# Optimization experiments

Hardware: AMD Instinct MI355X
Metric: run time of the kernel (lower is better)

## Reference

```python
import jax, jax.numpy as jnp
import numpy as np

SPATIAL_W = 1.0
INTENSITY_W = 1.0
MAX_ITERS = 100
CONV_THRESH = 1e-4
BOUNDARY = 0.1
NUM_CLASSES = 2
DIRS = ((-1, 0), (1, 0), (0, -1), (0, 1))  # 4-neighborhood


def setup_inputs() -> dict:
    key = jax.random.key(0)
    k1, k2, k3 = jax.random.split(key, 3)
    H = W = 1024
    image = jax.random.uniform(k1, (H, W), dtype=jnp.float32)
    labels = jax.random.randint(k2, (H, W), 1, NUM_CLASSES + 1)
    u = jax.random.uniform(k3, (H, W))
    seeds = jnp.where(u < 0.002, labels, 0).astype(jnp.int32)
    # guarantee both classes present (torch code maps sorted unique labels -> class idx)
    seeds = seeds.at[0, 0].set(1).at[0, 1].set(2)
    return {"image": image, "seeds": seeds}


def _shift(x, di, dj):
    """out[i, j] = x[i+di, j+dj] if in-bounds else 0. Static di, dj in {-1,0,1}."""
    H, W = x.shape[0], x.shape[1]
    pad = [(1, 1), (1, 1)] + [(0, 0)] * (x.ndim - 2)
    xp = jnp.pad(x, pad)
    return xp[1 + di:1 + di + H, 1 + dj:1 + dj + W]


def _transition_stencil(image):
    """Row-normalized 4-neighbor transition weights, [4, H, W].
    Equivalent to the dense NxN matrix P of the torch code restricted to its
    nonzero 4-neighbor stencil."""
    img = image[..., None]  # [H, W, 1] (grayscale -> C=1)
    ones = jnp.ones(image.shape, image.dtype)
    ws = []
    for di, dj in DIRS:
        valid = _shift(ones, di, dj)              # 1 where neighbor in-bounds
        nb = _shift(img, di, dj)                   # neighbor pixel values
        same = ((img > BOUNDARY) ^ (nb > BOUNDARY)).astype(image.dtype)
        diff = img - nb + same
        intensity = jnp.sqrt(jnp.sum(diff * diff, axis=-1))  # per-channel L2 norm
        dist = float(np.sqrt(di * di + dj * dj))  # == 1 for 4-neighborhood
        w = jnp.exp(-SPATIAL_W * dist) * jnp.exp(-INTENSITY_W * intensity) * valid
        ws.append(w)
    ws = jnp.stack(ws)  # [4, H, W]
    rowsum = jnp.sum(ws, axis=0)
    rowsum = jnp.where(rowsum == 0, jnp.ones_like(rowsum), rowsum)
    return ws / rowsum


def reference(image, seeds):
    P = _transition_stencil(image)  # [4, H, W]
    seed_mask = (seeds > 0)[..., None]  # [H, W, 1]
    # one-hot seed probabilities: label l -> class l-1 (sorted unique labels {1,2})
    init = jnp.stack([seeds == l for l in range(1, NUM_CLASSES + 1)],
                     axis=-1).astype(image.dtype)  # [H, W, C]

    def matvec(x):  # (P @ x) as a stencil: x is [H, W, C]
        out = jnp.zeros_like(x)
        for d, (di, dj) in enumerate(DIRS):
            out = out + P[d][..., None] * _shift(x, di, dj)
        return out

    def step(carry, _):
        x, done = carry
        new = jnp.where(seed_mask, init, matvec(x))  # seeds are absorbing
        d = jnp.linalg.norm(new - x)
        new = jnp.where(done, x, new)               # freeze after convergence
        done = done | (d < CONV_THRESH)
        return (new, done), None

    (x, _), _ = jax.lax.scan(step, (init, jnp.array(False)), None, length=MAX_ITERS)
    return x  # [H, W, NUM_CLASSES]
```

## Files before the change

kernel.cpp:

```cpp
#include <hip/hip_runtime.h>
#include <hip/hip_fp16.h>

typedef __attribute__((ext_vector_type(2))) int i32x2;

#define HH 1024
#define ROWP 512
#define NBLK 256
#define TPB 512
#define NSYNC 50
#define BOUNDARY_F 0.1f
#define TOKEN 0x5A5A5A5Au

union h2u { __half2 h; int i; };

__device__ __forceinline__ i32x2 pack4(float4 v) {
    h2u a, b;
    a.h = __float22half2_rn(make_float2(v.x, v.y));
    b.h = __float22half2_rn(make_float2(v.z, v.w));
    i32x2 r; r.x = a.i; r.y = b.i;
    return r;
}
__device__ __forceinline__ float4 unpack4(i32x2 p) {
    h2u a, b; a.i = p.x; b.i = p.y;
    float2 lo = __half22float2(a.h);
    float2 hi = __half22float2(b.h);
    return make_float4(lo.x, lo.y, hi.x, hi.y);
}

__device__ __forceinline__ void cst8(i32x2* base, int elem, i32x2 val) {
    asm volatile("global_store_dwordx2 %0, %1, %2 sc0 sc1"
                 :: "v"(elem * 8), "v"(val), "s"(base) : "memory");
}
__device__ __forceinline__ i32x2 cld8(const i32x2* base, int elem) {
    i32x2 t;
    asm volatile("global_load_dwordx2 %0, %1, %2 sc0 sc1"
                 : "=v"(t) : "v"(elem * 8), "s"(base) : "memory");
    return t;
}
__device__ __forceinline__ void wait4(i32x2& a, i32x2& b, i32x2& c, i32x2& d) {
    asm volatile("s_waitcnt vmcnt(0)"
                 : "+v"(a), "+v"(b), "+v"(c), "+v"(d) :: "memory");
}
__device__ __forceinline__ void waitvm0() {
    asm volatile("s_waitcnt vmcnt(0)" ::: "memory");
}

__device__ __forceinline__ float wfun(float c, float n, float valid) {
    float same = ((c > BOUNDARY_F) != (n > BOUNDARY_F)) ? 1.0f : 0.0f;
    return valid * __expf(-fabsf(c - n + same));
}

__device__ __forceinline__ float4 stepr(const float* w, bool m0, bool m1,
                                        float4 xc, float4 xu, float4 xd,
                                        float2 xl, float2 xr) {
    float4 o;
    o.x = w[0]*xu.x + w[1]*xd.x + w[2]*xl.x + w[3]*xc.z;
    o.y = w[0]*xu.y + w[1]*xd.y + w[2]*xl.y + w[3]*xc.w;
    o.z = w[4]*xu.z + w[5]*xd.z + w[6]*xc.x + w[7]*xr.x;
    o.w = w[4]*xu.w + w[5]*xd.w + w[6]*xc.y + w[7]*xr.y;
    if (m0) { o.x = xc.x; o.y = xc.y; }
    if (m1) { o.z = xc.z; o.w = xc.w; }
    return o;
}

__device__ __forceinline__ void horiz(const float4* row, int tid, float4 xc,
                                      float2* xl, float2* xr) {
    const float2* r2 = (const float2*)row;
    *xl = (tid > 0) ? r2[2 * tid - 1] : make_float2(xc.x, xc.y);
    *xr = (tid < ROWP - 1) ? r2[2 * tid + 2] : make_float2(xc.z, xc.w);
}

__launch_bounds__(TPB)
__global__ void rw_persist_kernel(const float* __restrict__ img,
                                  const int* __restrict__ seeds,
                                  float4* __restrict__ out4,
                                  i32x2* __restrict__ parE,
                                  i32x2* __restrict__ parO,
                                  unsigned* __restrict__ flags) {
    const int tid = threadIdx.x;
    const int blk = blockIdx.x;
    const int band = ((blk & 7) << 5) | (blk >> 3);
    const int i0 = band * 4;

    __shared__ float4 srows[10][ROWP];

    float cfv[6][8];
    unsigned mb0 = 0, mb1 = 0;
    float4 s0, s1, s2, s3;
    {
        const float2* img2 = (const float2*)img;
        const int2* seeds2 = (const int2*)seeds;
#pragma unroll
        for (int L = 0; L < 6; ++L) {
            const int g = min(max(i0 - 1 + L, 0), HH - 1);
            const int P = g * ROWP + tid;
            const int p = P * 2;
            const int j = p & 1023;
            const int uP = (g > 0) ? P - ROWP : P;
            const int dP = (g < HH - 1) ? P + ROWP : P;
            const int lp = (j > 0) ? p - 1 : p;
            const int rp = (j < 1022) ? p + 2 : p + 1;

            float2 cc = img2[P], iu = img2[uP], id = img2[dP];
            float il = img[lp], ir = img[rp];
            const float vU = (g > 0) ? 1.0f : 0.0f;
            const float vD = (g < HH - 1) ? 1.0f : 0.0f;
            const float vL = (j > 0) ? 1.0f : 0.0f;
            const float vR = (j < 1022) ? 1.0f : 0.0f;

            float w0u = wfun(cc.x, iu.x, vU), w0d = wfun(cc.x, id.x, vD);
            float w0l = wfun(cc.x, il, vL),   w0r = wfun(cc.x, cc.y, 1.0f);
            float rs0 = w0u + w0d + w0l + w0r;
            float inv0 = (rs0 > 0.0f) ? 1.0f / rs0 : 0.0f;
            float w1u = wfun(cc.y, iu.y, vU), w1d = wfun(cc.y, id.y, vD);
            float w1l = wfun(cc.y, cc.x, 1.0f), w1r = wfun(cc.y, ir, vR);
            float rs1 = w1u + w1d + w1l + w1r;
            float inv1 = (rs1 > 0.0f) ? 1.0f / rs1 : 0.0f;

            cfv[L][0] = w0u * inv0; cfv[L][1] = w0d * inv0;
            cfv[L][2] = w0l * inv0; cfv[L][3] = w0r * inv0;
            cfv[L][4] = w1u * inv1; cfv[L][5] = w1d * inv1;
            cfv[L][6] = w1l * inv1; cfv[L][7] = w1r * inv1;

            int2 s = seeds2[P];
            if (s.x > 0) mb0 |= 1u << L;
            if (s.y > 0) mb1 |= 1u << L;
            if (L >= 1 && L <= 4) {
                float4 v;
                v.x = (s.x == 1) ? 1.0f : 0.0f;
                v.y = (s.x == 2) ? 1.0f : 0.0f;
                v.z = (s.y == 1) ? 1.0f : 0.0f;
                v.w = (s.y == 2) ? 1.0f : 0.0f;
                if (L == 1) s0 = v; else if (L == 2) s1 = v;
                else if (L == 3) s2 = v; else s3 = v;
            }
        }
    }

    srows[1][tid] = s0; srows[2][tid] = s1;
    srows[3][tid] = s2; srows[4][tid] = s3;
    cst8(parE, (i0 + 0) * ROWP + tid, pack4(s0));
    cst8(parE, (i0 + 1) * ROWP + tid, pack4(s1));
    cst8(parE, (i0 + 2) * ROWP + tid, pack4(s2));
    cst8(parE, (i0 + 3) * ROWP + tid, pack4(s3));
    waitvm0();
    __syncthreads();
    if (tid == 0)
        __hip_atomic_store(&flags[band], TOKEN, __ATOMIC_RELAXED,
                           __HIP_MEMORY_SCOPE_AGENT);

    const int gU2 = max(i0 - 2, 0), gU1 = max(i0 - 1, 0);
    const int gD0 = min(i0 + 4, HH - 1), gD1 = min(i0 + 5, HH - 1);

    for (int m = 0; m < NSYNC; ++m) {
        if (tid == 0 && band > 0) {
            int guard = 0;
            while (__hip_atomic_load(&flags[m * NBLK + band - 1], __ATOMIC_RELAXED,
                                     __HIP_MEMORY_SCOPE_AGENT) != TOKEN) {
                __builtin_amdgcn_s_sleep(1);
                if (++guard > (1 << 20)) break;
            }
        }
        if (tid == 64 && band < NBLK - 1) {
            int guard = 0;
            while (__hip_atomic_load(&flags[m * NBLK + band + 1], __ATOMIC_RELAXED,
                                     __HIP_MEMORY_SCOPE_AGENT) != TOKEN) {
                __builtin_amdgcn_s_sleep(1);
                if (++guard > (1 << 20)) break;
            }
        }
        __syncthreads();
        asm volatile("" ::: "memory");

        const i32x2* pin = (m & 1) ? parO : parE;

        i32x2 rA = cld8(pin, gU2 * ROWP + tid);
        i32x2 rB = cld8(pin, gU1 * ROWP + tid);
        i32x2 rC = cld8(pin, gD0 * ROWP + tid);
        i32x2 rD = cld8(pin, gD1 * ROWP + tid);

        float2 xl, xr;
        horiz(&srows[2][0], tid, s1, &xl, &xr);
        float4 y2 = stepr(cfv[2], (mb0 >> 2) & 1, (mb1 >> 2) & 1, s1, s0, s2, xl, xr);
        horiz(&srows[3][0], tid, s2, &xl, &xr);
        float4 y3 = stepr(cfv[3], (mb0 >> 3) & 1, (mb1 >> 3) & 1, s2, s1, s3, xl, xr);
        srows[7][tid] = y2;
        srows[8][tid] = y3;

        wait4(rA, rB, rC, rD);
        float4 vU2 = unpack4(rA);
        float4 vU1 = unpack4(rB);
        float4 vD0 = unpack4(rC);
        float4 vD1 = unpack4(rD);
        srows[0][tid] = vU1;
        srows[5][tid] = vD0;
        __syncthreads();

        horiz(&srows[0][0], tid, vU1, &xl, &xr);
        float4 y0 = stepr(cfv[0], (mb0 >> 0) & 1, (mb1 >> 0) & 1, vU1, vU2, s0, xl, xr);
        horiz(&srows[1][0], tid, s0, &xl, &xr);
        float4 y1 = stepr(cfv[1], (mb0 >> 1) & 1, (mb1 >> 1) & 1, s0, vU1, s1, xl, xr);
        horiz(&srows[4][0], tid, s3, &xl, &xr);
        float4 y4 = stepr(cfv[4], (mb0 >> 4) & 1, (mb1 >> 4) & 1, s3, s2, vD0, xl, xr);
        horiz(&srows[5][0], tid, vD0, &xl, &xr);
        float4 y5 = stepr(cfv[5], (mb0 >> 5) & 1, (mb1 >> 5) & 1, vD0, s3, vD1, xl, xr);
        srows[6][tid] = y1;
        srows[9][tid] = y4;
        __syncthreads();

        horiz(&srows[6][0], tid, y1, &xl, &xr);
        float4 o0 = stepr(cfv[1], (mb0 >> 1) & 1, (mb1 >> 1) & 1, y1, y0, y2, xl, xr);
        horiz(&srows[7][0], tid, y2, &xl, &xr);
        float4 o1 = stepr(cfv[2], (mb0 >> 2) & 1, (mb1 >> 2) & 1, y2, y1, y3, xl, xr);
        horiz(&srows[8][0], tid, y3, &xl, &xr);
        float4 o2 = stepr(cfv[3], (mb0 >> 3) & 1, (mb1 >> 3) & 1, y3, y2, y4, xl, xr);
        horiz(&srows[9][0], tid, y4, &xl, &xr);
        float4 o3 = stepr(cfv[4], (mb0 >> 4) & 1, (mb1 >> 4) & 1, y4, y3, y5, xl, xr);

        if (m == NSYNC - 1) {
            out4[(i0 + 0) * ROWP + tid] = o0;
            out4[(i0 + 1) * ROWP + tid] = o1;
            out4[(i0 + 2) * ROWP + tid] = o2;
            out4[(i0 + 3) * ROWP + tid] = o3;
            break;
        }

        i32x2* pout = (m & 1) ? parE : parO;
        srows[1][tid] = o0; srows[2][tid] = o1;
        srows[3][tid] = o2; srows[4][tid] = o3;
        cst8(pout, (i0 + 0) * ROWP + tid, pack4(o0));
        cst8(pout, (i0 + 1) * ROWP + tid, pack4(o1));
        cst8(pout, (i0 + 2) * ROWP + tid, pack4(o2));
        cst8(pout, (i0 + 3) * ROWP + tid, pack4(o3));
        s0 = o0; s1 = o1; s2 = o2; s3 = o3;
        waitvm0();
        __syncthreads();
        if (tid == 0)
            __hip_atomic_store(&flags[(m + 1) * NBLK + band], TOKEN,
                               __ATOMIC_RELAXED, __HIP_MEMORY_SCOPE_AGENT);
    }
}

extern "C" void kernel_launch(void* const* d_in, const int* in_sizes, int n_in,
                              void* d_out, int out_size, void* d_ws, size_t ws_size,
                              hipStream_t stream) {
    const float* img = (const float*)d_in[0];
    const int* seeds = (const int*)d_in[1];

    float4* out4 = (float4*)d_out;
    char* ws = (char*)d_ws;
    i32x2* parE = (i32x2*)ws;
    i32x2* parO = (i32x2*)(ws + 4ull * 1024 * 1024);
    unsigned* flags = (unsigned*)(ws + 8ull * 1024 * 1024);

    rw_persist_kernel<<<NBLK, TPB, 0, stream>>>(img, seeds, out4, parE, parO, flags);
}
```

Measured before the change: 250.8 us.

## Switch from row bands to 2D tiles with shared-memory state and halo exchange

The persistent kernel now splits the grid into 16x16 two-dimensional tiles of 64x32 pixel-pairs instead of 4-row full-width bands. Tile state, coefficients and seed masks live in shared memory, and only halo cells are exchanged through global buffers. Each block waits on up to eight neighbour flags per sync step, and a separate init kernel clears the flags. The aim is to shrink global halo traffic per step relative to interior work. The cost is more LDS traffic and more synchronisation dependencies, plus an extra kernel launch.

```diff
diff --git a/kernel.cpp b/kernel.cpp
--- a/kernel.cpp
+++ b/kernel.cpp
@@ -1,15 +1,22 @@
 #include <hip/hip_runtime.h>
 #include <hip/hip_fp16.h>
 
+typedef unsigned long long u64;
 typedef __attribute__((ext_vector_type(2))) int i32x2;
 
 #define HH 1024
-#define ROWP 512
-#define NBLK 256
+#define WP 512
 #define TPB 512
+#define NTX 16
+#define NTY 16
+#define NBLK (NTX * NTY)
+#define SR 68
+#define SP 34
+#define NCELL (SR * SP)
 #define NSYNC 50
 #define BOUNDARY_F 0.1f
 #define TOKEN 0x5A5A5A5Au
+#define FLAGS_N (NSYNC * NBLK)
 
 union h2u { __half2 h; int i; };
 
@@ -20,27 +27,20 @@
     i32x2 r; r.x = a.i; r.y = b.i;
     return r;
 }
-__device__ __forceinline__ float4 unpack4(i32x2 p) {
-    h2u a, b; a.i = p.x; b.i = p.y;
+__device__ __forceinline__ float4 unpack4u(u64 p) {
+    h2u a, b; a.i = (int)(unsigned)p; b.i = (int)(unsigned)(p >> 32);
     float2 lo = __half22float2(a.h);
     float2 hi = __half22float2(b.h);
     return make_float4(lo.x, lo.y, hi.x, hi.y);
 }
 
+__device__ __forceinline__ u64 cld(const u64* p) {
+    return __hip_atomic_load(p, __ATOMIC_RELAXED, __HIP_MEMORY_SCOPE_AGENT);
+}
 __device__ __forceinline__ void cst8(i32x2* base, int elem, i32x2 val) {
     asm volatile("global_store_dwordx2 %0, %1, %2 sc0 sc1"
                  :: "v"(elem * 8), "v"(val), "s"(base) : "memory");
 }
-__device__ __forceinline__ i32x2 cld8(const i32x2* base, int elem) {
-    i32x2 t;
-    asm volatile("global_load_dwordx2 %0, %1, %2 sc0 sc1"
-                 : "=v"(t) : "v"(elem * 8), "s"(base) : "memory");
-    return t;
-}
-__device__ __forceinline__ void wait4(i32x2& a, i32x2& b, i32x2& c, i32x2& d) {
-    asm volatile("s_waitcnt vmcnt(0)"
-                 : "+v"(a), "+v"(b), "+v"(c), "+v"(d) :: "memory");
-}
 __device__ __forceinline__ void waitvm0() {
     asm volatile("s_waitcnt vmcnt(0)" ::: "memory");
 }
@@ -50,63 +50,63 @@
     return valid * __expf(-fabsf(c - n + same));
 }
 
-__device__ __forceinline__ float4 stepr(const float* w, bool m0, bool m1,
-                                        float4 xc, float4 xu, float4 xd,
-                                        float2 xl, float2 xr) {
+__device__ __forceinline__ float4 upd2(float4 c0, float4 c1, unsigned char m,
+                                       float4 xc, float4 xu, float4 xd,
+                                       float2 xl, float2 xr) {
     float4 o;
-    o.x = w[0]*xu.x + w[1]*xd.x + w[2]*xl.x + w[3]*xc.z;
-    o.y = w[0]*xu.y + w[1]*xd.y + w[2]*xl.y + w[3]*xc.w;
-    o.z = w[4]*xu.z + w[5]*xd.z + w[6]*xc.x + w[7]*xr.x;
-    o.w = w[4]*xu.w + w[5]*xd.w + w[6]*xc.y + w[7]*xr.y;
-    if (m0) { o.x = xc.x; o.y = xc.y; }
-    if (m1) { o.z = xc.z; o.w = xc.w; }
+    o.x = c0.x*xu.x + c0.y*xd.x + c0.z*xl.x + c0.w*xc.z;
+    o.y = c0.x*xu.y + c0.y*xd.y + c0.z*xl.y + c0.w*xc.w;
+    o.z = c1.x*xu.z + c1.y*xd.z + c1.z*xc.x + c1.w*xr.x;
+    o.w = c1.x*xu.w + c1.y*xd.w + c1.z*xc.y + c1.w*xr.y;
+    if (m & 1) { o.x = xc.x; o.y = xc.y; }
+    if (m & 2) { o.z = xc.z; o.w = xc.w; }
     return o;
 }
 
-__device__ __forceinline__ void horiz(const float4* row, int tid, float4 xc,
-                                      float2* xl, float2* xr) {
-    const float2* r2 = (const float2*)row;
-    *xl = (tid > 0) ? r2[2 * tid - 1] : make_float2(xc.x, xc.y);
-    *xr = (tid < ROWP - 1) ? r2[2 * tid + 2] : make_float2(xc.z, xc.w);
+__global__ void rw_init_kernel(unsigned* __restrict__ flags) {
+    int g = blockIdx.x * blockDim.x + threadIdx.x;
+    if (g < FLAGS_N) flags[g] = 0u;
 }
 
 __launch_bounds__(TPB)
 __global__ void rw_persist_kernel(const float* __restrict__ img,
                                   const int* __restrict__ seeds,
                                   float4* __restrict__ out4,
-                                  i32x2* __restrict__ parE,
-                                  i32x2* __restrict__ parO,
+                                  u64* __restrict__ parE,
+                                  u64* __restrict__ parO,
                                   unsigned* __restrict__ flags) {
     const int tid = threadIdx.x;
     const int blk = blockIdx.x;
-    const int band = ((blk & 7) << 5) | (blk >> 3);
-    const int i0 = band * 4;
-
-    __shared__ float4 srows[10][ROWP];
-
-    float cfv[6][8];
-    unsigned mb0 = 0, mb1 = 0;
-    float4 s0, s1, s2, s3;
+    const int tx = blk & (NTX - 1), ty = blk >> 4;
+    const int row0 = ty * 64 - 2;
+    const int pr0  = tx * 32 - 1;
+
+    __shared__ float4 xs[SR][SP + 1];
+    __shared__ float4 cf0s[SR][SP];
+    __shared__ float4 cf1s[SR][SP];
+    __shared__ unsigned char msks[SR][SP + 2];
+
     {
         const float2* img2 = (const float2*)img;
         const int2* seeds2 = (const int2*)seeds;
-#pragma unroll
-        for (int L = 0; L < 6; ++L) {
-            const int g = min(max(i0 - 1 + L, 0), HH - 1);
-            const int P = g * ROWP + tid;
-            const int p = P * 2;
-            const int j = p & 1023;
-            const int uP = (g > 0) ? P - ROWP : P;
-            const int dP = (g < HH - 1) ? P + ROWP : P;
-            const int lp = (j > 0) ? p - 1 : p;
-            const int rp = (j < 1022) ? p + 2 : p + 1;
+        for (int c = tid; c < NCELL; c += TPB) {
+            const int r = c / SP, q = c - (c / SP) * SP;
+            const int gi = row0 + r;
+            const int gq = pr0 + q;
+            const int ci = min(max(gi, 0), HH - 1);
+            const int cq = min(max(gq, 0), WP - 1);
+            const int gj = 2 * gq;
+            const int P  = ci * WP + cq;
+            const int uP = max(ci - 1, 0) * WP + cq;
+            const int dP = min(ci + 1, HH - 1) * WP + cq;
 
             float2 cc = img2[P], iu = img2[uP], id = img2[dP];
-            float il = img[lp], ir = img[rp];
-            const float vU = (g > 0) ? 1.0f : 0.0f;
-            const float vD = (g < HH - 1) ? 1.0f : 0.0f;
-            const float vL = (j > 0) ? 1.0f : 0.0f;
-            const float vR = (j < 1022) ? 1.0f : 0.0f;
+            float il = img[max(2 * P - 1, 0)];
+            float ir = img[min(2 * P + 2, HH * 1024 - 1)];
+            const float vU = (gi > 0) ? 1.0f : 0.0f;
+            const float vD = (gi < HH - 1) ? 1.0f : 0.0f;
+            const float vL = (gj > 0) ? 1.0f : 0.0f;
+            const float vR = (gj < 1022) ? 1.0f : 0.0f;
 
             float w0u = wfun(cc.x, iu.x, vU), w0d = wfun(cc.x, id.x, vD);
             float w0l = wfun(cc.x, il, vL),   w0r = wfun(cc.x, cc.y, 1.0f);
@@ -117,126 +117,142 @@
             float rs1 = w1u + w1d + w1l + w1r;
             float inv1 = (rs1 > 0.0f) ? 1.0f / rs1 : 0.0f;
 
-            cfv[L][0] = w0u * inv0; cfv[L][1] = w0d * inv0;
-            cfv[L][2] = w0l * inv0; cfv[L][3] = w0r * inv0;
-            cfv[L][4] = w1u * inv1; cfv[L][5] = w1d * inv1;
-            cfv[L][6] = w1l * inv1; cfv[L][7] = w1r * inv1;
+            cf0s[r][q] = make_float4(w0u*inv0, w0d*inv0, w0l*inv0, w0r*inv0);
+            cf1s[r][q] = make_float4(w1u*inv1, w1d*inv1, w1l*inv1, w1r*inv1);
 
             int2 s = seeds2[P];
-            if (s.x > 0) mb0 |= 1u << L;
-            if (s.y > 0) mb1 |= 1u << L;
-            if (L >= 1 && L <= 4) {
-                float4 v;
-                v.x = (s.x == 1) ? 1.0f : 0.0f;
-                v.y = (s.x == 2) ? 1.0f : 0.0f;
-                v.z = (s.y == 1) ? 1.0f : 0.0f;
-                v.w = (s.y == 2) ? 1.0f : 0.0f;
-                if (L == 1) s0 = v; else if (L == 2) s1 = v;
-                else if (L == 3) s2 = v; else s3 = v;
-            }
+            msks[r][q] = (unsigned char)((s.x > 0 ? 1 : 0) | (s.y > 0 ? 2 : 0));
+            xs[r][q] = make_float4((s.x == 1) ? 1.0f : 0.0f,
+                                   (s.x == 2) ? 1.0f : 0.0f,
+                                   (s.y == 1) ? 1.0f : 0.0f,
+                                   (s.y == 2) ? 1.0f : 0.0f);
         }
     }
-
-    srows[1][tid] = s0; srows[2][tid] = s1;
-    srows[3][tid] = s2; srows[4][tid] = s3;
-    cst8(parE, (i0 + 0) * ROWP + tid, pack4(s0));
-    cst8(parE, (i0 + 1) * ROWP + tid, pack4(s1));
-    cst8(parE, (i0 + 2) * ROWP + tid, pack4(s2));
-    cst8(parE, (i0 + 3) * ROWP + tid, pack4(s3));
-    waitvm0();
     __syncthreads();
-    if (tid == 0)
-        __hip_atomic_store(&flags[band], TOKEN, __ATOMIC_RELAXED,
-                           __HIP_MEMORY_SCOPE_AGENT);
-
-    const int gU2 = max(i0 - 2, 0), gU1 = max(i0 - 1, 0);
-    const int gD0 = min(i0 + 4, HH - 1), gD1 = min(i0 + 5, HH - 1);
+
+    int sr = 0, sq = 0;
+    const bool isStager = (tid < 264);
+    if (tid < 136) {
+        int k = tid / SP;
+        sr = (k < 2) ? k : 64 + k;
+        sq = tid - k * SP;
+    } else if (tid < 264) {
+        int j = tid - 136;
+        sr = 2 + (j >> 1);
+        sq = (j & 1) * 33;
+    }
+    const int sgi = min(max(row0 + sr, 0), HH - 1);
+    const int sgq = min(max(pr0 + sq, 0), WP - 1);
 
     for (int m = 0; m < NSYNC; ++m) {
-        if (tid == 0 && band > 0) {
-            int guard = 0;
-            while (__hip_atomic_load(&flags[m * NBLK + band - 1], __ATOMIC_RELAXED,
-                                     __HIP_MEMORY_SCOPE_AGENT) != TOKEN) {
-                __builtin_amdgcn_s_sleep(1);
-                if (++guard > (1 << 20)) break;
-            }
-        }
-        if (tid == 64 && band < NBLK - 1) {
-            int guard = 0;
-            while (__hip_atomic_load(&flags[m * NBLK + band + 1], __ATOMIC_RELAXED,
-                                     __HIP_MEMORY_SCOPE_AGENT) != TOKEN) {
-                __builtin_amdgcn_s_sleep(1);
-                if (++guard > (1 << 20)) break;
-            }
-        }
-        __syncthreads();
-        asm volatile("" ::: "memory");
-
-        const i32x2* pin = (m & 1) ? parO : parE;
-
-        i32x2 rA = cld8(pin, gU2 * ROWP + tid);
-        i32x2 rB = cld8(pin, gU1 * ROWP + tid);
-        i32x2 rC = cld8(pin, gD0 * ROWP + tid);
-        i32x2 rD = cld8(pin, gD1 * ROWP + tid);
-
-        float2 xl, xr;
-        horiz(&srows[2][0], tid, s1, &xl, &xr);
-        float4 y2 = stepr(cfv[2], (mb0 >> 2) & 1, (mb1 >> 2) & 1, s1, s0, s2, xl, xr);
-        horiz(&srows[3][0], tid, s2, &xl, &xr);
-        float4 y3 = stepr(cfv[3], (mb0 >> 3) & 1, (mb1 >> 3) & 1, s2, s1, s3, xl, xr);
-        srows[7][tid] = y2;
-        srows[8][tid] = y3;
-
-        wait4(rA, rB, rC, rD);
-        float4 vU2 = unpack4(rA);
-        float4 vU1 = unpack4(rB);
-        float4 vD0 = unpack4(rC);
-        float4 vD1 = unpack4(rD);
-        srows[0][tid] = vU1;
-        srows[5][tid] = vD0;
-        __syncthreads();
-
-        horiz(&srows[0][0], tid, vU1, &xl, &xr);
-        float4 y0 = stepr(cfv[0], (mb0 >> 0) & 1, (mb1 >> 0) & 1, vU1, vU2, s0, xl, xr);
-        horiz(&srows[1][0], tid, s0, &xl, &xr);
-        float4 y1 = stepr(cfv[1], (mb0 >> 1) & 1, (mb1 >> 1) & 1, s0, vU1, s1, xl, xr);
-        horiz(&srows[4][0], tid, s3, &xl, &xr);
-        float4 y4 = stepr(cfv[4], (mb0 >> 4) & 1, (mb1 >> 4) & 1, s3, s2, vD0, xl, xr);
-        horiz(&srows[5][0], tid, vD0, &xl, &xr);
-        float4 y5 = stepr(cfv[5], (mb0 >> 5) & 1, (mb1 >> 5) & 1, vD0, s3, vD1, xl, xr);
-        srows[6][tid] = y1;
-        srows[9][tid] = y4;
-        __syncthreads();
-
-        horiz(&srows[6][0], tid, y1, &xl, &xr);
-        float4 o0 = stepr(cfv[1], (mb0 >> 1) & 1, (mb1 >> 1) & 1, y1, y0, y2, xl, xr);
-        horiz(&srows[7][0], tid, y2, &xl, &xr);
-        float4 o1 = stepr(cfv[2], (mb0 >> 2) & 1, (mb1 >> 2) & 1, y2, y1, y3, xl, xr);
-        horiz(&srows[8][0], tid, y3, &xl, &xr);
-        float4 o2 = stepr(cfv[3], (mb0 >> 3) & 1, (mb1 >> 3) & 1, y3, y2, y4, xl, xr);
-        horiz(&srows[9][0], tid, y4, &xl, &xr);
-        float4 o3 = stepr(cfv[4], (mb0 >> 4) & 1, (mb1 >> 4) & 1, y4, y3, y5, xl, xr);
+        u64 stg = 0;
+        if (m > 0) {
+            if (tid < 8) {
+                const int dy[8] = {-1, 1, 0, 0, -1, -1, 1, 1};
+                const int dx[8] = {0, 0, -1, 1, -1, 1, -1, 1};
+                int nty = ty + dy[tid], ntx = tx + dx[tid];
+                if (nty >= 0 && nty < NTY && ntx >= 0 && ntx < NTX) {
+                    const int fi = m * NBLK + nty * NTX + ntx;
+                    int guard = 0;
+                    while (__hip_atomic_load(&flags[fi], __ATOMIC_RELAXED,
+                                             __HIP_MEMORY_SCOPE_AGENT) != TOKEN) {
+                        __builtin_amdgcn_s_sleep(1);
+                        if (++guard > (1 << 20)) break;
+                    }
+                }
+            }
+            __syncthreads();
+            asm volatile("" ::: "memory");
+            const u64* pin = (m & 1) ? parO : parE;
+            if (isStager) stg = cld(&pin[sgi * WP + sgq]);
+        }
+
+        float4 yA[4];
+#pragma unroll
+        for (int k = 0; k < 4; ++k) {
+            int idx = tid + k * TPB;
+            if (idx < 1860) {
+                int r = 3 + idx / 30, q = 2 + idx % 30;
+                float4 xc = xs[r][q];
+                float2 xl = make_float2(xs[r][q - 1].z, xs[r][q - 1].w);
+                float2 xr = make_float2(xs[r][q + 1].x, xs[r][q + 1].y);
+                yA[k] = upd2(cf0s[r][q], cf1s[r][q], msks[r][q],
+                             xc, xs[r - 1][q], xs[r + 1][q], xl, xr);
+            }
+        }
+        if (m > 0 && isStager) xs[sr][sq] = unpack4u(stg);
+        __syncthreads();
+
+        float4 yB;
+        int br = 1, bq = 0;
+        if (tid < 384) {
+            if (tid < 136) {
+                int k = tid / SP;
+                br = (k < 2) ? 1 + k : 63 + k;
+                bq = tid - k * SP;
+            } else {
+                int j = tid - 136;
+                br = 3 + (j >> 2);
+                const int QT[4] = {0, 1, 32, 33};
+                bq = QT[j & 3];
+            }
+            float4 xc = xs[br][bq];
+            float2 xl = (bq > 0) ? make_float2(xs[br][bq - 1].z, xs[br][bq - 1].w)
+                                 : make_float2(xc.x, xc.y);
+            float2 xr = (bq < SP - 1) ? make_float2(xs[br][bq + 1].x, xs[br][bq + 1].y)
+                                      : make_float2(xc.z, xc.w);
+            yB = upd2(cf0s[br][bq], cf1s[br][bq], msks[br][bq],
+                      xc, xs[br - 1][bq], xs[br + 1][bq], xl, xr);
+        }
+        __syncthreads();
+
+#pragma unroll
+        for (int k = 0; k < 4; ++k) {
+            int idx = tid + k * TPB;
+            if (idx < 1860) {
+                int r = 3 + idx / 30, q = 2 + idx % 30;
+                xs[r][q] = yA[k];
+            }
+        }
+        if (tid < 384) xs[br][bq] = yB;
+        __syncthreads();
+
+        float4 o[4];
+#pragma unroll
+        for (int k = 0; k < 4; ++k) {
+            int c = tid + k * TPB;
+            int r = 2 + (c >> 5), q = 1 + (c & 31);
+            float4 xc = xs[r][q];
+            float2 xl = make_float2(xs[r][q - 1].z, xs[r][q - 1].w);
+            float2 xr = make_float2(xs[r][q + 1].x, xs[r][q + 1].y);
+            o[k] = upd2(cf0s[r][q], cf1s[r][q], msks[r][q],
+                        xc, xs[r - 1][q], xs[r + 1][q], xl, xr);
+        }
 
         if (m == NSYNC - 1) {
-            out4[(i0 + 0) * ROWP + tid] = o0;
-            out4[(i0 + 1) * ROWP + tid] = o1;
-            out4[(i0 + 2) * ROWP + tid] = o2;
-            out4[(i0 + 3) * ROWP + tid] = o3;
+#pragma unroll
+            for (int k = 0; k < 4; ++k) {
+                int c = tid + k * TPB;
+                int r = 2 + (c >> 5), q = 1 + (c & 31);
+                out4[(row0 + r) * WP + (pr0 + q)] = o[k];
+            }
             break;
         }
 
-        i32x2* pout = (m & 1) ? parE : parO;
-        srows[1][tid] = o0; srows[2][tid] = o1;
-        srows[3][tid] = o2; srows[4][tid] = o3;
-        cst8(pout, (i0 + 0) * ROWP + tid, pack4(o0));
-        cst8(pout, (i0 + 1) * ROWP + tid, pack4(o1));
-        cst8(pout, (i0 + 2) * ROWP + tid, pack4(o2));
-        cst8(pout, (i0 + 3) * ROWP + tid, pack4(o3));
-        s0 = o0; s1 = o1; s2 = o2; s3 = o3;
+        __syncthreads();
+        i32x2* pout = (i32x2*)(((m + 1) & 1) ? parO : parE);
+#pragma unroll
+        for (int k = 0; k < 4; ++k) {
+            int c = tid + k * TPB;
+            int r = 2 + (c >> 5), q = 1 + (c & 31);
+            xs[r][q] = o[k];
+            if (r <= 3 || r >= 64 || q == 1 || q == 32)
+                cst8(pout, (row0 + r) * WP + (pr0 + q), pack4(o[k]));
+        }
         waitvm0();
         __syncthreads();
         if (tid == 0)
-            __hip_atomic_store(&flags[(m + 1) * NBLK + band], TOKEN,
+            __hip_atomic_store(&flags[(m + 1) * NBLK + blk], TOKEN,
                                __ATOMIC_RELAXED, __HIP_MEMORY_SCOPE_AGENT);
     }
 }
@@ -249,9 +265,10 @@
 
     float4* out4 = (float4*)d_out;
     char* ws = (char*)d_ws;
-    i32x2* parE = (i32x2*)ws;
-    i32x2* parO = (i32x2*)(ws + 4ull * 1024 * 1024);
+    u64* parE = (u64*)ws;
+    u64* parO = (u64*)(ws + 4ull * 1024 * 1024);
     unsigned* flags = (unsigned*)(ws + 8ull * 1024 * 1024);
 
+    rw_init_kernel<<<(FLAGS_N + 255) / 256, 256, 0, stream>>>(flags);
     rw_persist_kernel<<<NBLK, TPB, 0, stream>>>(img, seeds, out4, parE, parO, flags);
 }
```

Result: slower. 346.6 us (+38.2%).
